# Performance work log

Measured on AMD Instinct MI355X. Metric: run time of the kernel, lower is better.

The kernel has to match this reference:

```python
import jax, jax.numpy as jnp
import numpy as np

D_ENC = 768
D_MS = 64
N_LAYERS = 3
EPS = 1e-5

def setup_inputs() -> dict:
    key = jax.random.key(0)
    k1, k2 = jax.random.split(key)
    x = jax.random.normal(k1, (8, 2304, D_ENC), dtype=jnp.float32)
    Wq = jax.random.normal(k2, (D_ENC, D_MS), dtype=jnp.float32) * (D_ENC ** -0.5)
    bq = jnp.zeros((D_MS,), dtype=jnp.float32)
    gamma = jnp.ones((D_ENC,), dtype=jnp.float32)
    beta = jnp.zeros((D_ENC,), dtype=jnp.float32)
    return {"x": x, "Wq": Wq, "bq": bq, "gamma": gamma, "beta": beta}

def _layer_norm(x, gamma, beta):
    mu = jnp.mean(x, axis=-1, keepdims=True)
    var = jnp.mean(jnp.square(x - mu), axis=-1, keepdims=True)
    return (x - mu) * jax.lax.rsqrt(var + EPS) * gamma + beta

def reference(x, Wq, bq, gamma, beta):
    scale = D_MS ** -0.5
    for _ in range(N_LAYERS):
        q = jnp.einsum('bnd,dm->bnm', x, Wq) + bq          # [B,N,Dm]
        sim = jnp.einsum('bnm,bkm->bnk', q, q) * scale     # [B,N,N]
        attn = jax.nn.softmax(sim, axis=-1)
        x = jnp.einsum('bnk,bkd->bnd', attn, x)            # [B,N,D]
        x = _layer_norm(x, gamma, beta)
    return x
```

## Files before the change

### kernel.cpp

```cpp
#include <hip/hip_runtime.h>
#include <math.h>

#define BB 8
#define NN 2304
#define DD 768
#define DM 64
#define EPSF 1e-5f

typedef __attribute__((ext_vector_type(8))) short short8;
typedef __attribute__((ext_vector_type(4))) short short4v;
typedef __attribute__((ext_vector_type(4))) float f32x4;
typedef __attribute__((ext_vector_type(2))) unsigned int uint2v;

static __device__ __forceinline__ unsigned short f2b(float f) {
    unsigned u = __float_as_uint(f);
    unsigned r = u + 0x7FFFu + ((u >> 16) & 1u);
    return (unsigned short)(r >> 16);
}
static __device__ __forceinline__ float b2f(unsigned short h) {
    return __uint_as_float(((unsigned)h) << 16);
}
#define MFMA(a, b, c) __builtin_amdgcn_mfma_f32_16x16x32_bf16((a), (b), (c), 0, 0, 0)

__global__ __launch_bounds__(256) void cvt_kernel(const float* __restrict__ xf,
                                                  unsigned short* __restrict__ xTh,
                                                  unsigned short* __restrict__ xTl) {
    __shared__ __align__(16) unsigned short Th[64][72];
    __shared__ __align__(16) unsigned short Tl[64][72];
    int t = threadIdx.x;
    int b = blockIdx.z;
    int n0 = blockIdx.x * 64, c0 = blockIdx.y * 64;
    int rr = t >> 4, cc = (t & 15) * 4;
    #pragma unroll
    for (int i = 0; i < 4; ++i) {
        int r = rr + i * 16;
        long idx = ((long)b * NN + n0 + r) * DD + c0 + cc;
        float4 v = *(const float4*)&xf[idx];
        unsigned short h0 = f2b(v.x), h1 = f2b(v.y), h2 = f2b(v.z), h3 = f2b(v.w);
        Th[cc + 0][r] = h0; Th[cc + 1][r] = h1; Th[cc + 2][r] = h2; Th[cc + 3][r] = h3;
        Tl[cc + 0][r] = f2b(v.x - b2f(h0));
        Tl[cc + 1][r] = f2b(v.y - b2f(h1));
        Tl[cc + 2][r] = f2b(v.z - b2f(h2));
        Tl[cc + 3][r] = f2b(v.w - b2f(h3));
    }
    __syncthreads();
    #pragma unroll
    for (int i = 0; i < 4; ++i) {
        int c = rr + i * 16;
        long idx = ((long)b * DD + c0 + c) * NN + n0 + cc;
        *(ushort4*)&xTh[idx] = *(const ushort4*)&Th[c][cc];
        *(ushort4*)&xTl[idx] = *(const ushort4*)&Tl[c][cc];
    }
}

__global__ __launch_bounds__(256) void wqcvt_kernel(const float* __restrict__ Wq,
                                                    unsigned short* __restrict__ Wth,
                                                    unsigned short* __restrict__ Wtl) {
    int t = blockIdx.x * 256 + threadIdx.x;
    int d = t >> 6, m = t & 63;
    float v = Wq[t];
    unsigned short h = f2b(v);
    Wth[m * DD + d] = h;
    Wtl[m * DD + d] = f2b(v - b2f(h));
}

__global__ __launch_bounds__(256) void zstats_kernel(float* __restrict__ stats) {
    stats[blockIdx.x * 256 + threadIdx.x] = 0.f;
}

__global__ __launch_bounds__(256) void proj_kernel(
        const unsigned short* __restrict__ Wth, const unsigned short* __restrict__ Wtl,
        const unsigned short* __restrict__ xTh, const unsigned short* __restrict__ xTl,
        const float* __restrict__ bq,
        unsigned short* __restrict__ qh, unsigned short* __restrict__ ql) {
    int t = threadIdx.x;
    int w = t >> 6, lane = t & 63, quad = lane >> 4, l15 = lane & 15;
    int n0 = blockIdx.x * 64, b = blockIdx.y;
    const unsigned short* xhb = xTh + (long)b * DD * NN;
    const unsigned short* xlb = xTl + (long)b * DD * NN;

    f32x4 accQ[4];
    #pragma unroll
    for (int nt = 0; nt < 4; ++nt) accQ[nt] = 0.f;

    for (int d0 = 0; d0 < DD; d0 += 32) {
        short8 ah = *(const short8*)&Wth[(w * 16 + l15) * DD + d0 + quad * 8];
        short8 al = *(const short8*)&Wtl[(w * 16 + l15) * DD + d0 + quad * 8];
        #pragma unroll
        for (int nt = 0; nt < 4; ++nt) {
            int row = n0 + nt * 16 + l15;
            short8 bh, bl;
            #pragma unroll
            for (int j = 0; j < 8; ++j) {
                long o = (long)(d0 + quad * 8 + j) * NN + row;
                bh[j] = (short)xhb[o];
                bl[j] = (short)xlb[o];
            }
            accQ[nt] = MFMA(ah, bh, accQ[nt]);
            accQ[nt] = MFMA(al, bh, accQ[nt]);
            accQ[nt] = MFMA(ah, bl, accQ[nt]);
        }
    }
    #pragma unroll
    for (int nt = 0; nt < 4; ++nt) {
        int row = n0 + nt * 16 + l15;
        #pragma unroll
        for (int e = 0; e < 4; ++e) {
            int qm = w * 16 + quad * 4 + e;
            float v = accQ[nt][e] + bq[qm];
            unsigned short h = f2b(v);
            long o = ((long)b * NN + row) * DM + qm;
            qh[o] = h;
            ql[o] = f2b(v - b2f(h));
        }
    }
}

__global__ __launch_bounds__(256) void qk_kernel(
        const unsigned short* __restrict__ qhp, const unsigned short* __restrict__ qlp,
        unsigned short* __restrict__ Ph, unsigned short* __restrict__ Pl,
        float* __restrict__ lsumG, int bofs) {
    const int t = threadIdx.x;
    const int w = t >> 6, lane = t & 63, quad = lane >> 4, l15 = lane & 15;
    const int sk = w & 1, sr = w >> 1;
    const int n0 = blockIdx.x * 96;
    const int k00 = blockIdx.y * 576;
    const int bL = blockIdx.z, b = bofs + bL;
    const unsigned short* qhb = qhp + (long)b * NN * DM;
    const unsigned short* qlb = qlp + (long)b * NN * DM;

    short8 bh[3][2], bl[3][2];
    #pragma unroll
    for (int rt = 0; rt < 3; ++rt)
        #pragma unroll
        for (int kc = 0; kc < 2; ++kc) {
            long o = (long)(n0 + sr * 48 + rt * 16 + l15) * DM + kc * 32 + quad * 8;
            bh[rt][kc] = *(const short8*)(qhb + o);
            bl[rt][kc] = *(const short8*)(qlb + o);
        }
    float lp[3] = {0.f, 0.f, 0.f};

    for (int k0 = k00; k0 < k00 + 576; k0 += 64) {
        #pragma unroll
        for (int kt = 0; kt < 2; ++kt) {
            long ao = (long)(k0 + sk * 32 + kt * 16 + l15) * DM + quad * 8;
            short8 qh0 = *(const short8*)(qhb + ao);
            short8 qh1 = *(const short8*)(qhb + ao + 32);
            short8 ql0 = *(const short8*)(qlb + ao);
            short8 ql1 = *(const short8*)(qlb + ao + 32);
            #pragma unroll
            for (int rt = 0; rt < 3; ++rt) {
                f32x4 s = 0.f;
                s = MFMA(qh0, bh[rt][0], s);
                s = MFMA(qh1, bh[rt][1], s);
                s = MFMA(ql0, bh[rt][0], s);
                s = MFMA(ql1, bh[rt][1], s);
                s = MFMA(qh0, bl[rt][0], s);
                s = MFMA(qh1, bl[rt][1], s);
                float p0 = __expf(s[0] * 0.125f);
                float p1 = __expf(s[1] * 0.125f);
                float p2 = __expf(s[2] * 0.125f);
                float p3 = __expf(s[3] * 0.125f);
                lp[rt] += (p0 + p1) + (p2 + p3);
                unsigned u0 = __float_as_uint(p0), u1 = __float_as_uint(p1);
                unsigned u2 = __float_as_uint(p2), u3 = __float_as_uint(p3);
                uint2v dh = { (u0 >> 16) | (u1 & 0xFFFF0000u),
                              (u2 >> 16) | (u3 & 0xFFFF0000u) };
                float r0 = p0 - __uint_as_float(u0 & 0xFFFF0000u);
                float r1 = p1 - __uint_as_float(u1 & 0xFFFF0000u);
                float r2 = p2 - __uint_as_float(u2 & 0xFFFF0000u);
                float r3 = p3 - __uint_as_float(u3 & 0xFFFF0000u);
                unsigned v0 = __float_as_uint(r0), v1 = __float_as_uint(r1);
                unsigned v2 = __float_as_uint(r2), v3 = __float_as_uint(r3);
                uint2v dl = { (v0 >> 16) | (v1 & 0xFFFF0000u),
                              (v2 >> 16) | (v3 & 0xFFFF0000u) };
                int row = n0 + sr * 48 + rt * 16 + l15;
                long po = ((long)bL * NN + row) * NN + k0 + sk * 32 + kt * 16 + quad * 4;
                *(uint2v*)&Ph[po] = dh;
                *(uint2v*)&Pl[po] = dl;
            }
        }
    }
    #pragma unroll
    for (int rt = 0; rt < 3; ++rt) {
        float v = lp[rt];
        v += __shfl_xor(v, 16); v += __shfl_xor(v, 32);
        if (lane < 16)
            atomicAdd(&lsumG[(long)b * NN + n0 + sr * 48 + rt * 16 + l15], v);
    }
}

__global__ __launch_bounds__(256, 3) void pv_kernel(
        const unsigned short* __restrict__ Ph, const unsigned short* __restrict__ Pl,
        const unsigned short* __restrict__ xTh, const unsigned short* __restrict__ xTl,
        const float* __restrict__ lsumG, float* __restrict__ OT,
        float* __restrict__ stats, int bofs) {
    __shared__ __align__(16) unsigned short SM[2][4][3072];
    const int t = threadIdx.x;
    const int w = t >> 6, lane = t & 63, quad = lane >> 4, l15 = lane & 15;
    const int wc = w & 1, wr = w >> 1;
    const int cb = blockIdx.x * 96;
    const int n0 = blockIdx.y * 96;
    const int bL = blockIdx.z, b = bofs + bL;
    const unsigned short* xhb = xTh + (long)b * DD * NN;
    const unsigned short* xlb = xTl + (long)b * DD * NN;
    const unsigned short* phb = Ph + (long)bL * NN * NN;
    const unsigned short* plb = Pl + (long)bL * NN * NN;
    const unsigned short* srcArr = (w == 0) ? xhb : (w == 1) ? xlb
                                 : (w == 2) ? phb : plb;
    const int rbg = (w < 2) ? cb : n0;
    const int rl0 = lane >> 2, sl = lane & 3;

    f32x4 acc[3][3];
    #pragma unroll
    for (int ct = 0; ct < 3; ++ct)
        #pragma unroll
        for (int nt = 0; nt < 3; ++nt) acc[ct][nt] = 0.f;

#define STAGE(BUF_, K0_) do {                                                      \
    _Pragma("unroll")                                                              \
    for (int j = 0; j < 6; ++j) {                                                  \
        int rowL = j * 16 + rl0;                                                   \
        int koct = sl ^ ((rowL >> 1) & 3);                                         \
        __builtin_amdgcn_global_load_lds(                                          \
            (const __attribute__((address_space(1))) void*)                        \
                (srcArr + (long)(rbg + rowL) * NN + (K0_) + koct * 8),             \
            (__attribute__((address_space(3))) void*)&SM[BUF_][w][j * 512],        \
            16, 0, 0);                                                             \
    }                                                                              \
} while (0)

    STAGE(0, 0);
    for (int ph = 0; ph < NN / 32; ++ph) {
        const int buf = ph & 1;
        __builtin_amdgcn_s_barrier();
        {
            int kn = (ph + 1) * 32; if (kn >= NN) kn = 0;
            STAGE(buf ^ 1, kn);
        }
        asm volatile("s_waitcnt vmcnt(6)" ::: "memory");
        __builtin_amdgcn_s_barrier();
        __builtin_amdgcn_sched_barrier(0);
        __builtin_amdgcn_s_setprio(1);
        {
            short8 pbh[3], pbl[3];
            #pragma unroll
            for (int nt = 0; nt < 3; ++nt) {
                int rl = wr * 48 + nt * 16 + l15;
                int so = rl * 32 + ((quad ^ ((rl >> 1) & 3)) * 8);
                pbh[nt] = *(const short8*)&SM[buf][2][so];
                pbl[nt] = *(const short8*)&SM[buf][3][so];
            }
            #pragma unroll
            for (int ct = 0; ct < 3; ++ct) {
                int cl = wc * 48 + ct * 16 + l15;
                int so = cl * 32 + ((quad ^ ((cl >> 1) & 3)) * 8);
                short8 axh = *(const short8*)&SM[buf][0][so];
                short8 axl = *(const short8*)&SM[buf][1][so];
                #pragma unroll
                for (int nt = 0; nt < 3; ++nt) {
                    acc[ct][nt] = MFMA(axh, pbh[nt], acc[ct][nt]);
                    acc[ct][nt] = MFMA(axl, pbh[nt], acc[ct][nt]);
                    acc[ct][nt] = MFMA(axh, pbl[nt], acc[ct][nt]);
                }
            }
        }
        __builtin_amdgcn_s_setprio(0);
    }
#undef STAGE

    float* OTb = OT + (long)b * DD * NN;
    #pragma unroll
    for (int nt = 0; nt < 3; ++nt) {
        int rowl = wr * 48 + nt * 16 + l15;
        int row = n0 + rowl;
        float linv = 1.f / lsumG[(long)b * NN + row];
        float s1 = 0.f, s2 = 0.f;
        #pragma unroll
        for (int ct = 0; ct < 3; ++ct)
            #pragma unroll
            for (int e = 0; e < 4; ++e) {
                float vv = acc[ct][nt][e] * linv;
                acc[ct][nt][e] = vv;
                s1 += vv; s2 += vv * vv;
            }
        s1 += __shfl_xor(s1, 16); s1 += __shfl_xor(s1, 32);
        s2 += __shfl_xor(s2, 16); s2 += __shfl_xor(s2, 32);
        #pragma unroll
        for (int ct = 0; ct < 3; ++ct)
            #pragma unroll
            for (int e = 0; e < 4; ++e)
                OTb[(long)(cb + wc * 48 + ct * 16 + quad * 4 + e) * NN + row] =
                    acc[ct][nt][e];
        if (lane < 16) {
            atomicAdd(&stats[((long)b * NN + row) * 2 + 0], s1);
            atomicAdd(&stats[((long)b * NN + row) * 2 + 1], s2);
        }
    }
}

#define ATTN_SETUP                                                                  \
    const int t = threadIdx.x;                                                      \
    const int w = t >> 6, lane = t & 63, quad = lane >> 4, l15 = lane & 15;         \
    const int bx = blockIdx.x;                                                      \
    const int combo = bx & 63, rt_idx = bx >> 6;                                    \
    const int b = combo & 7, g = combo >> 3;                                        \
    const int n0 = rt_idx * 96;                                                     \
    const int cb = g * 96;                                                          \
    const int sk = w & 1, sr = w >> 1;                                              \
    const int pbase = w * 1536;                                                     \
    if (t < 96) lsum[t] = 0.f;                                                      \
    const unsigned short* qhb = qhp + (long)b * NN * DM;                            \
    const unsigned short* qlb = qlp + (long)b * NN * DM;                            \
    const unsigned short* xhb = xTh + (long)b * DD * NN;                            \
    const unsigned short* xlb = xTl + (long)b * DD * NN;                            \
    short8 bh[3][2], bl[3][2];                                                      \
    _Pragma("unroll")                                                               \
    for (int rt = 0; rt < 3; ++rt) {                                                \
        _Pragma("unroll")                                                           \
        for (int kc = 0; kc < 2; ++kc) {                                            \
            long o = (long)(n0 + sr * 48 + rt * 16 + l15) * DM + kc * 32 + quad * 8;\
            bh[rt][kc] = *(const short8*)(qhb + o);                                 \
            bl[rt][kc] = *(const short8*)(qlb + o);                                 \
        }                                                                           \
    }                                                                               \
    float lp[3] = {0.f, 0.f, 0.f};                                                  \
    f32x4 acc[6][3];                                                                \
    _Pragma("unroll")                                                               \
    for (int ct = 0; ct < 6; ++ct) {                                                \
        _Pragma("unroll")                                                           \
        for (int nt = 0; nt < 3; ++nt) acc[ct][nt] = 0.f;                           \
    }

#define DMA_X(DH_, DL_, KB_) do {                                                   \
    _Pragma("unroll")                                                               \
    for (int j = 0; j < 6; ++j) {                                                   \
        int cg = w * 6 + j;                                                         \
        int cm = cg - (cg >= 12 ? 12 : 0);                                          \
        unsigned short* dstb = (cg < 12 ? (DH_) : (DL_)) + cm * 512;                \
        const unsigned short* srcb = (cg < 12 ? xhb : xlb);                         \
        int col = cm * 8 + (lane >> 3);                                             \
        int key = ((lane & 7) ^ (col & 7)) * 8;                                     \
        __builtin_amdgcn_global_load_lds(                                           \
            (const __attribute__((address_space(1))) void*)                         \
                (srcb + (long)(cb + col) * NN + (KB_) + key),                       \
            (__attribute__((address_space(3))) void*)dstb, 16, 0, 0);               \
    }                                                                               \
} while (0)

#define QPF(QN_, KQ_) do {                                                          \
    _Pragma("unroll")                                                               \
    for (int kt = 0; kt < 2; ++kt) {                                                \
        long o = (long)((KQ_) + sk * 32 + kt * 16 + l15) * DM + quad * 8;           \
        QN_[kt * 4 + 0] = *(const short8*)(qhb + o);                                \
        QN_[kt * 4 + 1] = *(const short8*)(qhb + o + 32);                           \
        QN_[kt * 4 + 2] = *(const short8*)(qlb + o);                                \
        QN_[kt * 4 + 3] = *(const short8*)(qlb + o + 32);                           \
    }                                                                               \
} while (0)

#define S_KT(QH0_, QH1_, QL0_, QL1_, KT_) do {                                      \
    _Pragma("unroll")                                                               \
    for (int rt = 0; rt < 3; ++rt) {                                                \
        f32x4 s = 0.f;                                                              \
        s = MFMA(QH0_, bh[rt][0], s);                                               \
        s = MFMA(QH1_, bh[rt][1], s);                                               \
        s = MFMA(QL0_, bh[rt][0], s);                                               \
        s = MFMA(QL1_, bh[rt][1], s);                                               \
        s = MFMA(QH0_, bl[rt][0], s);                                               \
        s = MFMA(QH1_, bl[rt][1], s);                                               \
        float p0 = __expf(s[0] * 0.125f);                                           \
        float p1 = __expf(s[1] * 0.125f);                                           \
        float p2 = __expf(s[2] * 0.125f);                                           \
        float p3 = __expf(s[3] * 0.125f);                                           \
        lp[rt] += (p0 + p1) + (p2 + p3);                                            \
        unsigned u0 = __float_as_uint(p0), u1 = __float_as_uint(p1);                \
        unsigned u2 = __float_as_uint(p2), u3 = __float_as_uint(p3);                \
        uint2v dh = { (u0 >> 16) | (u1 & 0xFFFF0000u),                              \
                      (u2 >> 16) | (u3 & 0xFFFF0000u) };                            \
        float r0 = p0 - __uint_as_float(u0 & 0xFFFF0000u);                          \
        float r1 = p1 - __uint_as_float(u1 & 0xFFFF0000u);                          \
        float r2 = p2 - __uint_as_float(u2 & 0xFFFF0000u);                          \
        float r3 = p3 - __uint_as_float(u3 & 0xFFFF0000u);                          \
        unsigned v0 = __float_as_uint(r0), v1 = __float_as_uint(r1);                \
        unsigned v2 = __float_as_uint(r2), v3 = __float_as_uint(r3);                \
        uint2v dl = { (v0 >> 16) | (v1 & 0xFFFF0000u),                              \
                      (v2 >> 16) | (v3 & 0xFFFF0000u) };                            \
        int rr_ = rt * 16 + l15;                                                    \
        int ff_ = (((rr_ & 7) ^ (rr_ >> 3)) & 7) << 2;                              \
        int ix_ = pbase + rr_ * 32 + (((KT_) * 16 + quad * 4) ^ ff_);               \
        *(uint2v*)&PHs[ix_] = dh;                                                   \
        *(uint2v*)&PLs[ix_] = dl;                                                   \
    }                                                                               \
} while (0)

#define PV_PHASE(XH_, XL_) do {                                                     \
    short8 pbh[3], pbl[3];                                                          \
    _Pragma("unroll")                                                               \
    for (int nt = 0; nt < 3; ++nt) {                                                \
        int r_ = nt * 16 + l15;                                                     \
        int ff_ = (((r_ & 7) ^ (r_ >> 3)) & 7) << 2;                                \
        int i0 = pbase + r_ * 32 + ((quad * 8) ^ ff_);                              \
        int i1 = pbase + r_ * 32 + ((quad * 8 + 4) ^ ff_);                          \
        short4v h0 = *(const short4v*)&PHs[i0];                                     \
        short4v h1 = *(const short4v*)&PHs[i1];                                     \
        short4v l0 = *(const short4v*)&PLs[i0];                                     \
        short4v l1 = *(const short4v*)&PLs[i1];                                     \
        pbh[nt] = __builtin_shufflevector(h0, h1, 0, 1, 2, 3, 4, 5, 6, 7);          \
        pbl[nt] = __builtin_shufflevector(l0, l1, 0, 1, 2, 3, 4, 5, 6, 7);          \
    }                                                                               \
    _Pragma("unroll")                                                               \
    for (int ct = 0; ct < 6; ++ct) {                                                \
        int colx = ct * 16 + l15;                                                   \
        int xk = (sk * 32 + quad * 8) ^ ((colx & 7) << 3);                          \
        short8 axh = *(const short8*)&(XH_)[colx * 64 + xk];                        \
        short8 axl = *(const short8*)&(XL_)[colx * 64 + xk];                        \
        _Pragma("unroll")                                                           \
        for (int nt = 0; nt < 3; ++nt) {                                            \
            acc[ct][nt] = MFMA(axh, pbh[nt], acc[ct][nt]);                          \
            acc[ct][nt] = MFMA(axl, pbh[nt], acc[ct][nt]);                          \
            acc[ct][nt] = MFMA(axh, pbl[nt], acc[ct][nt]);                          \
        }                                                                           \
    }                                                                               \
} while (0)

#define ATTN_EPILOGUE do {                                                          \
    _Pragma("unroll")                                                               \
    for (int rt = 0; rt < 3; ++rt) {                                                \
        float v = lp[rt];                                                           \
        v += __shfl_xor(v, 16); v += __shfl_xor(v, 32);                             \
        if (lane < 16) atomicAdd(&lsum[sr * 48 + rt * 16 + l15], v);                \
    }                                                                               \
    float* M = (float*)SMEM;                                                        \
    __syncthreads();                                                                \
    if (sk == 1) {                                                                  \
        float* Mw = M + sr * (48 * 100);                                            \
        _Pragma("unroll")                                                           \
        for (int nt = 0; nt < 3; ++nt) {                                            \
            _Pragma("unroll")                                                       \
            for (int ct = 0; ct < 6; ++ct)                                          \
                *(f32x4*)&Mw[(nt * 16 + l15) * 100 + ct * 16 + quad * 4] = acc[ct][nt]; \
        }                                                                           \
    }                                                                               \
    __syncthreads();                                                                \
    if (sk == 0) {                                                                  \
        const float* Mr = M + sr * (48 * 100);                                      \
        float* OTb = OT + (long)b * DD * NN;                                        \
        _Pragma("unroll")                                                           \
        for (int nt = 0; nt < 3; ++nt) {                                            \
            int rowl = sr * 48 + nt * 16 + l15;                                     \
            int row = n0 + rowl;                                                    \
            float linv = 1.f / lsum[rowl];                                          \
            float s1 = 0.f, s2 = 0.f;                                               \
            _Pragma("unroll")                                                       \
            for (int ct = 0; ct < 6; ++ct) {                                        \
                f32x4 pq = *(const f32x4*)&Mr[(nt * 16 + l15) * 100 + ct * 16 + quad * 4]; \
                _Pragma("unroll")                                                   \
                for (int e = 0; e < 4; ++e) {                                       \
                    float vv = (acc[ct][nt][e] + pq[e]) * linv;                     \
                    acc[ct][nt][e] = vv;                                            \
                    s1 += vv; s2 += vv * vv;                                        \
                }                                                                   \
            }                                                                       \
            s1 += __shfl_xor(s1, 16); s1 += __shfl_xor(s1, 32);                     \
            s2 += __shfl_xor(s2, 16); s2 += __shfl_xor(s2, 32);                     \
            _Pragma("unroll")                                                       \
            for (int ct = 0; ct < 6; ++ct) {                                        \
                _Pragma("unroll")                                                   \
                for (int e = 0; e < 4; ++e)                                         \
                    OTb[(long)(cb + ct * 16 + quad * 4 + e) * NN + row] = acc[ct][nt][e]; \
            }                                                                       \
            if (lane < 16) {                                                        \
                atomicAdd(&stats[((long)b * NN + row) * 2 + 0], s1);                \
                atomicAdd(&stats[((long)b * NN + row) * 2 + 1], s2);                \
            }                                                                       \
        }                                                                           \
    }                                                                               \
} while (0)

__global__ __launch_bounds__(256, 2) void attn_v0(
        const unsigned short* __restrict__ qhp, const unsigned short* __restrict__ qlp,
        const unsigned short* __restrict__ xTh, const unsigned short* __restrict__ xTl,
        float* __restrict__ OT, float* __restrict__ stats) {
    __shared__ __align__(16) unsigned char SMEM[49536];
    unsigned short* XHs = (unsigned short*)SMEM;
    unsigned short* XLs = XHs + 6144;
    unsigned short* PHs = XHs + 12288;
    unsigned short* PLs = XHs + 18432;
    float* lsum = (float*)(SMEM + 49152);
    ATTN_SETUP;
    short8 qA[8], qB[8];
    QPF(qA, 0);
    for (int kp = 0; kp < NN; kp += 128) {
        __syncthreads();
        DMA_X(XHs, XLs, kp);
        { int kq = kp + 64; QPF(qB, kq); }
        S_KT(qA[0], qA[1], qA[2], qA[3], 0);
        S_KT(qA[4], qA[5], qA[6], qA[7], 1);
        __syncthreads();
        __builtin_amdgcn_s_setprio(1);
        PV_PHASE(XHs, XLs);
        __builtin_amdgcn_s_setprio(0);
        __syncthreads();
        DMA_X(XHs, XLs, kp + 64);
        { int kq = kp + 128; if (kq >= NN) kq = 0; QPF(qA, kq); }
        S_KT(qB[0], qB[1], qB[2], qB[3], 0);
        S_KT(qB[4], qB[5], qB[6], qB[7], 1);
        __syncthreads();
        __builtin_amdgcn_s_setprio(1);
        PV_PHASE(XHs, XLs);
        __builtin_amdgcn_s_setprio(0);
    }
    ATTN_EPILOGUE;
}

__global__ __launch_bounds__(256) void lncvt_mid_kernel(
        const float* __restrict__ OT, const float* __restrict__ stats,
        const float* __restrict__ gamma, const float* __restrict__ beta,
        unsigned short* __restrict__ xTh, unsigned short* __restrict__ xTl) {
    int t = threadIdx.x;
    int n = blockIdx.x * 64 + (t & 63);
    int b = blockIdx.z;
    int c0 = blockIdx.y * 192 + (t >> 6);
    float s1 = stats[((long)b * NN + n) * 2 + 0];
    float s2 = stats[((long)b * NN + n) * 2 + 1];
    float mu = s1 * (1.f / 768.f);
    float rs = rsqrtf(s2 * (1.f / 768.f) - mu * mu + EPSF);
    const float* OTb = OT + (long)b * DD * NN;
    #pragma unroll 4
    for (int i = 0; i < 48; ++i) {
        int c = c0 + i * 4;
        float o = OTb[(long)c * NN + n];
        float y = (o - mu) * rs * gamma[c] + beta[c];
        unsigned short h = f2b(y);
        long idx = ((long)b * DD + c) * NN + n;
        xTh[idx] = h;
        xTl[idx] = f2b(y - b2f(h));
    }
}

__global__ __launch_bounds__(256) void lncvt_final_kernel(
        const float* __restrict__ OT, const float* __restrict__ stats,
        const float* __restrict__ gamma, const float* __restrict__ beta,
        float* __restrict__ out) {
    __shared__ float T[64][65];
    int t = threadIdx.x;
    int nl = t & 63, cw = t >> 6;
    int b = blockIdx.y, n0 = blockIdx.x * 64;
    int n = n0 + nl;
    float s1 = stats[((long)b * NN + n) * 2 + 0];
    float s2 = stats[((long)b * NN + n) * 2 + 1];
    float mu = s1 * (1.f / 768.f);
    float rs = rsqrtf(s2 * (1.f / 768.f) - mu * mu + EPSF);
    const float* OTb = OT + (long)b * DD * NN;
    float* ob = out + (long)b * NN * DD;
    int row_l = t >> 2, seg = t & 3;
    for (int ct = 0; ct < 12; ++ct) {
        #pragma unroll
        for (int i = 0; i < 16; ++i) {
            int cl = cw + i * 4;
            int c = ct * 64 + cl;
            float o = OTb[(long)c * NN + n];
            T[nl][cl] = (o - mu) * rs * gamma[c] + beta[c];
        }
        __syncthreads();
        #pragma unroll
        for (int i = 0; i < 4; ++i) {
            int cl = seg * 16 + i * 4;
            float4 v = *(const float4*)&T[row_l][cl];
            *(float4*)&ob[(long)(n0 + row_l) * DD + ct * 64 + cl] = v;
        }
        __syncthreads();
    }
}

extern "C" void kernel_launch(void* const* d_in, const int* in_sizes, int n_in,
                              void* d_out, int out_size, void* d_ws, size_t ws_size,
                              hipStream_t stream) {
    (void)in_sizes; (void)n_in; (void)out_size;
    const float* x     = (const float*)d_in[0];
    const float* Wq    = (const float*)d_in[1];
    const float* bq    = (const float*)d_in[2];
    const float* gamma = (const float*)d_in[3];
    const float* beta  = (const float*)d_in[4];
    float* out = (float*)d_out;

    char* p = (char*)d_ws;
    const size_t szXT = (size_t)BB * DD * NN * 2;
    unsigned short* xTh = (unsigned short*)p; p += szXT;
    unsigned short* xTl = (unsigned short*)p; p += szXT;
    float* OT           = (float*)p;          p += (size_t)BB * DD * NN * 4;
    unsigned short* qh  = (unsigned short*)p; p += (size_t)BB * NN * DM * 2;
    unsigned short* ql  = (unsigned short*)p; p += (size_t)BB * NN * DM * 2;
    float* stats        = (float*)p;          p += (size_t)BB * NN * 2 * 4;
    float* lsumG        = (float*)p;          p += (size_t)BB * NN * 4;
    unsigned short* Wth = (unsigned short*)p; p += (size_t)DM * DD * 2;
    unsigned short* Wtl = (unsigned short*)p; p += (size_t)DM * DD * 2;

    size_t used = (size_t)(p - (char*)d_ws);
    const size_t perB = (size_t)NN * NN * 2 * 2;
    int gb = 0;
    if      (ws_size >= used + 8 * perB) gb = 8;
    else if (ws_size >= used + 4 * perB) gb = 4;
    else if (ws_size >= used + 2 * perB) gb = 2;
    else if (ws_size >= used + 1 * perB) gb = 1;
    unsigned short* Ph = (unsigned short*)p;
    unsigned short* Pl = Ph + (size_t)(gb > 0 ? gb : 1) * NN * NN;

    cvt_kernel<<<dim3(NN / 64, DD / 64, BB), 256, 0, stream>>>(x, xTh, xTl);
    wqcvt_kernel<<<dim3(DD * DM / 256), 256, 0, stream>>>(Wq, Wth, Wtl);

    for (int layer = 0; layer < 3; ++layer) {
        proj_kernel<<<dim3(NN / 64, BB), 256, 0, stream>>>(Wth, Wtl, xTh, xTl, bq, qh, ql);
        zstats_kernel<<<dim3(BB * NN * 3 / 256), 256, 0, stream>>>(stats);
        if (gb > 0) {
            for (int g0 = 0; g0 < BB; g0 += gb) {
                qk_kernel<<<dim3(NN / 96, 4, gb), 256, 0, stream>>>(
                    qh, ql, Ph, Pl, lsumG, g0);
                pv_kernel<<<dim3(DD / 96, NN / 96, gb), 256, 0, stream>>>(
                    Ph, Pl, xTh, xTl, lsumG, OT, stats, g0);
            }
        } else {
            attn_v0<<<dim3(24 * 64), 256, 0, stream>>>(qh, ql, xTh, xTl, OT, stats);
        }
        if (layer < 2)
            lncvt_mid_kernel<<<dim3(NN / 64, 4, BB), 256, 0, stream>>>(OT, stats, gamma, beta, xTh, xTl);
        else
            lncvt_final_kernel<<<dim3(NN / 64, BB), 256, 0, stream>>>(OT, stats, gamma, beta, out);
    }
}
```

Baseline: 1.379 ms.

## Stage P tiles through swizzled LDS for wide stores; remap pv blocks for XCD locality

The qk kernel now writes its bf16 hi/lo probability fragments into XOR-swizzled shared memory per wave, then reads them back and writes 16-byte contiguous chunks per row to global memory, replacing scattered 8-byte stores. The pv kernel changes to a 1D grid with a remapping that sends the 8 column blocks for a given row block to the same XCD slot (phys & 7), so they can share the P tile in L2. The cost is extra LDS traffic and some added index arithmetic.

New measurement: 1.226 ms. 11.1% less time.

```diff
diff --git a/kernel.cpp b/kernel.cpp
--- a/kernel.cpp
+++ b/kernel.cpp
@@ -120,9 +120,12 @@
         const unsigned short* __restrict__ qhp, const unsigned short* __restrict__ qlp,
         unsigned short* __restrict__ Ph, unsigned short* __restrict__ Pl,
         float* __restrict__ lsumG, int bofs) {
+    __shared__ __align__(16) unsigned short PHs[4 * 1536];
+    __shared__ __align__(16) unsigned short PLs[4 * 1536];
     const int t = threadIdx.x;
     const int w = t >> 6, lane = t & 63, quad = lane >> 4, l15 = lane & 15;
     const int sk = w & 1, sr = w >> 1;
+    const int pbase = w * 1536;
     const int n0 = blockIdx.x * 96;
     const int k00 = blockIdx.y * 576;
     const int bL = blockIdx.z, b = bofs + bL;
@@ -174,11 +177,29 @@
                 unsigned v2 = __float_as_uint(r2), v3 = __float_as_uint(r3);
                 uint2v dl = { (v0 >> 16) | (v1 & 0xFFFF0000u),
                               (v2 >> 16) | (v3 & 0xFFFF0000u) };
-                int row = n0 + sr * 48 + rt * 16 + l15;
-                long po = ((long)bL * NN + row) * NN + k0 + sk * 32 + kt * 16 + quad * 4;
-                *(uint2v*)&Ph[po] = dh;
-                *(uint2v*)&Pl[po] = dl;
+                int rr = rt * 16 + l15;
+                int ff = (((rr & 7) ^ (rr >> 3)) & 7) << 2;
+                int ix = pbase + rr * 32 + ((kt * 16 + quad * 4) ^ ff);
+                *(uint2v*)&PHs[ix] = dh;
+                *(uint2v*)&PLs[ix] = dl;
             }
+        }
+        #pragma unroll
+        for (int r = 0; r < 3; ++r) {
+            int c = r * 64 + lane;
+            int rr = c >> 2, s = c & 3;
+            int ff = (((rr & 7) ^ (rr >> 3)) & 7) << 2;
+            int i0 = pbase + rr * 32 + ((s * 8) ^ ff);
+            int i1 = pbase + rr * 32 + ((s * 8 + 4) ^ ff);
+            short4v h0 = *(const short4v*)&PHs[i0];
+            short4v h1 = *(const short4v*)&PHs[i1];
+            short4v l0 = *(const short4v*)&PLs[i0];
+            short4v l1 = *(const short4v*)&PLs[i1];
+            short8 hh = __builtin_shufflevector(h0, h1, 0, 1, 2, 3, 4, 5, 6, 7);
+            short8 ll = __builtin_shufflevector(l0, l1, 0, 1, 2, 3, 4, 5, 6, 7);
+            long po = ((long)bL * NN + n0 + sr * 48 + rr) * NN + k0 + sk * 32 + s * 8;
+            *(short8*)&Ph[po] = hh;
+            *(short8*)&Pl[po] = ll;
         }
     }
     #pragma unroll
@@ -199,9 +220,14 @@
     const int t = threadIdx.x;
     const int w = t >> 6, lane = t & 63, quad = lane >> 4, l15 = lane & 15;
     const int wc = w & 1, wr = w >> 1;
-    const int cb = blockIdx.x * 96;
-    const int n0 = blockIdx.y * 96;
-    const int bL = blockIdx.z, b = bofs + bL;
+    const int phys = blockIdx.x;
+    const int gc = phys & 7;
+    const int inner = phys >> 3;
+    const int m = inner & 7;
+    const int g = ((inner >> 3) << 3) + gc;
+    const int cb = m * 96;
+    const int n0 = (g % 24) * 96;
+    const int bL = g / 24, b = bofs + bL;
     const unsigned short* xhb = xTh + (long)b * DD * NN;
     const unsigned short* xlb = xTl + (long)b * DD * NN;
     const unsigned short* phb = Ph + (long)bL * NN * NN;
@@ -617,7 +643,7 @@
             for (int g0 = 0; g0 < BB; g0 += gb) {
                 qk_kernel<<<dim3(NN / 96, 4, gb), 256, 0, stream>>>(
                     qh, ql, Ph, Pl, lsumG, g0);
-                pv_kernel<<<dim3(DD / 96, NN / 96, gb), 256, 0, stream>>>(
+                pv_kernel<<<dim3(8 * (NN / 96) * gb), 256, 0, stream>>>(
                     Ph, Pl, xTh, xTl, lsumG, OT, stats, g0);
             }
         } else {
```
